# Optimization experiments

Measured on AMD Instinct MI355X. Metric: run time of the kernel, lower is better.

## Reference

```python
import jax, jax.numpy as jnp
import numpy as np

N = 16384            # mesh vertices at full resolution (level 3)
DEG = 8              # avg nonzeros per Laplacian row
F_IN = 3
F_HID = 128
LOCAL_LAYERS = 15
LEVEL_N = [N >> (3 - l) for l in range(4)]  # [2048, 4096, 8192, 16384]


def setup_inputs():
    key = jax.random.key(0)
    ks = iter(jax.random.split(key, 48))
    d = {}
    d['inputs'] = jax.random.normal(next(ks), (1, N, F_IN), dtype=jnp.float32)
    d['mask0'] = jnp.ones((1, N, 1), jnp.float32)
    d['mask1'] = jnp.ones((1, N, 1), jnp.float32)
    for l, n in enumerate(LEVEL_N):
        e = DEG * n
        d[f'lap{l}_rows'] = jnp.sort(jax.random.randint(next(ks), (e,), 0, n, dtype=jnp.int32))
        d[f'lap{l}_cols'] = jax.random.randint(next(ks), (e,), 0, n, dtype=jnp.int32)
        d[f'lap{l}_vals'] = 0.25 * jax.random.normal(next(ks), (e,), dtype=jnp.float32)
    e = DEG * N
    d['L_rows'] = jnp.sort(jax.random.randint(next(ks), (e,), 0, N, dtype=jnp.int32))
    d['L_cols'] = jax.random.randint(next(ks), (e,), 0, N, dtype=jnp.int32)
    d['L_vals'] = 0.25 * jax.random.normal(next(ks), (e,), dtype=jnp.float32)
    s_in = 0.577   # ~1/sqrt(F_IN)
    s_h = 0.0625   # 1/sqrt(2*F_HID)
    d['g_conv1_W'] = s_in * jax.random.normal(next(ks), (F_IN, F_HID), dtype=jnp.float32)
    d['g_conv1_b'] = jnp.zeros((F_HID,), jnp.float32)
    d['g_down_W'] = s_h * jax.random.normal(next(ks), (3, 2, 2 * F_HID, F_HID), dtype=jnp.float32)
    d['g_down_b'] = jnp.zeros((3, 2, F_HID), jnp.float32)
    d['g_lap0_W'] = s_h * jax.random.normal(next(ks), (2, 2 * F_HID, F_HID), dtype=jnp.float32)
    d['g_lap0_b'] = jnp.zeros((2, F_HID), jnp.float32)
    d['g_up_W'] = s_h * jax.random.normal(next(ks), (3, 2, 2 * F_HID, F_HID), dtype=jnp.float32)
    d['g_up_b'] = jnp.zeros((3, 2, F_HID), jnp.float32)
    d['g_conv2_W'] = s_h * jax.random.normal(next(ks), (F_HID, 2), dtype=jnp.float32)
    d['g_conv2_b'] = jnp.zeros((2,), jnp.float32)
    d['l_conv1_W'] = s_in * jax.random.normal(next(ks), (F_IN, F_HID), dtype=jnp.float32)
    d['l_conv1_b'] = jnp.zeros((F_HID,), jnp.float32)
    d['l_rn_W'] = s_h * jax.random.normal(next(ks), (LOCAL_LAYERS, 2, 2 * F_HID, F_HID), dtype=jnp.float32)
    d['l_rn_b'] = jnp.zeros((LOCAL_LAYERS, 2, F_HID), jnp.float32)
    d['l_conv2_W'] = s_h * jax.random.normal(next(ks), (F_HID, 1), dtype=jnp.float32)
    d['l_conv2_b'] = jnp.zeros((1,), jnp.float32)
    return d


def _spmm(rows, cols, vals, x):
    # y = L @ x for an n x n COO Laplacian; x: [1, n, f] (batch=1, sparse mm path)
    y = jax.ops.segment_sum(vals[:, None] * x[0, cols, :], rows, num_segments=x.shape[1])
    return y[None]


def _lap_block(lap, x, Ws, bs):
    # _LapResNet2 (num_outputs == num_inputs == 128): elu -> cat([x, Lx]) -> 1x1 conv, residual
    inp = x
    for j in range(Ws.shape[0]):
        x = jax.nn.elu(x)
        x = jnp.concatenate([x, _spmm(lap[0], lap[1], lap[2], x)], axis=-1) @ Ws[j] + bs[j]
    return x + inp


def _avg_block(mask, x, Ws, bs):
    # _AvgResNet2: elu -> cat([x, masked global average]) -> 1x1 conv, residual
    inp = x
    denom = jnp.sum(mask, axis=1, keepdims=True)
    for j in range(Ws.shape[0]):
        x = jax.nn.elu(x)
        avg = jnp.sum(x * mask, axis=1, keepdims=True) / denom
        x = jnp.concatenate([x, jnp.broadcast_to(avg, x.shape)], axis=-1) @ Ws[j] + bs[j]
    return x + inp


def _maxpool2(x):
    # MaxPool1d(2, stride=2) along the node dim
    b, n, f = x.shape
    return x.reshape(b, n // 2, 2, f).max(axis=2)


def _forward(inputs, mask0, mask1, lap0_vals, lap1_vals, lap2_vals, lap3_vals, L_vals,
             g_conv1_W, g_conv1_b, g_down_W, g_down_b, g_lap0_W, g_lap0_b,
             g_up_W, g_up_b, g_conv2_W, g_conv2_b,
             l_conv1_W, l_conv1_b, l_rn_W, l_rn_b, l_conv2_W, l_conv2_b,
             lap0_rows, lap0_cols, lap1_rows, lap1_cols, lap2_rows, lap2_cols,
             lap3_rows, lap3_cols, L_rows, L_cols):
    laps = [(lap0_rows, lap0_cols, lap0_vals), (lap1_rows, lap1_cols, lap1_vals),
            (lap2_rows, lap2_cols, lap2_vals), (lap3_rows, lap3_cols, lap3_vals)]
    # ----- global net: EfficientCascade (naive max-pool cascade, 4 levels) -----
    # (mask0 is only max-pooled in torch; _LapResNet2 ignores it, so it does not affect math)
    x = inputs @ g_conv1_W + g_conv1_b
    down = []
    for k, i in enumerate((3, 2, 1)):
        down.append(x)
        x = _lap_block(laps[i], x, g_down_W[k], g_down_b[k])
        x = _maxpool2(x)
    x = _lap_block(laps[0], x, g_lap0_W, g_lap0_b)
    for i in (1, 2, 3):
        x = jnp.repeat(x, 2, axis=1)      # F.interpolate(scale_factor=2), nearest
        x = x + down[-i]                  # channels equal -> plain residual add
        x = _lap_block(laps[i], x, g_up_W[i - 1], g_up_b[i - 1])
    swg = jax.nn.elu(x) @ g_conv2_W + g_conv2_b + inputs[:, :, :2]  # + repeating_expand(inputs, 2)
    # ----- local net: LapDeepModel, 15 alternating Lap / global-avg resblocks -----
    L = (L_rows, L_cols, L_vals)
    y = inputs @ l_conv1_W + l_conv1_b
    for i in range(LOCAL_LAYERS):
        if i % 2 == 0:
            y = _lap_block(L, y, l_rn_W[i], l_rn_b[i])
        else:
            y = _avg_block(mask1, y, l_rn_W[i], l_rn_b[i])
    score_local = jax.nn.elu(y) @ l_conv2_W + l_conv2_b + inputs[:, :, :1]
    # ----- combine -----
    score_global = swg[:, :, :1]
    weight_global = jax.nn.sigmoid(swg[:, :, :-1])  # out_features=1 -> same first channel
    score_final = weight_global * score_global + (1.0 - weight_global) * score_local
    return jnp.concatenate([score_global, score_local, score_final], axis=1)


def reference(inputs, mask0, mask1, lap0_rows, lap0_cols, lap0_vals,
              lap1_rows, lap1_cols, lap1_vals, lap2_rows, lap2_cols, lap2_vals,
              lap3_rows, lap3_cols, lap3_vals, L_rows, L_cols, L_vals,
              g_conv1_W, g_conv1_b, g_down_W, g_down_b, g_lap0_W, g_lap0_b,
              g_up_W, g_up_b, g_conv2_W, g_conv2_b,
              l_conv1_W, l_conv1_b, l_rn_W, l_rn_b, l_conv2_W, l_conv2_b):
    return _forward(inputs, mask0, mask1, lap0_vals, lap1_vals, lap2_vals, lap3_vals, L_vals,
                    g_conv1_W, g_conv1_b, g_down_W, g_down_b, g_lap0_W, g_lap0_b,
                    g_up_W, g_up_b, g_conv2_W, g_conv2_b,
                    l_conv1_W, l_conv1_b, l_rn_W, l_rn_b, l_conv2_W, l_conv2_b,
                    lap0_rows, lap0_cols, lap1_rows, lap1_cols, lap2_rows, lap2_cols,
                    lap3_rows, lap3_cols, L_rows, L_cols)
```

## Files before the change

### kernel.cpp

```cpp
#include <hip/hip_runtime.h>

#define F 128
#define SPAD 136
#define NR 32

typedef __attribute__((ext_vector_type(8))) short short8;
typedef __attribute__((ext_vector_type(16))) float f32x16;
typedef unsigned long long ull;

__device__ __forceinline__ float elu_f(float x) {
    return x > 0.f ? x : __expf(x) - 1.f;
}
__device__ __forceinline__ ushort f2bf(float x) {
    unsigned u = __float_as_uint(x);
    u = (u + 0x7FFFu + ((u >> 16) & 1u)) >> 16;
    return (ushort)u;
}
__device__ __forceinline__ float bf2f(ushort u) {
    return __uint_as_float((unsigned)u << 16);
}
__device__ __forceinline__ void bfma8(float* a, float v, short8 u) {
#pragma unroll
    for (int i = 0; i < 8; ++i) a[i] += v * bf2f((ushort)u[i]);
}

struct SetupArgs {
    const float* ws0; const float* ws1; const float* ws2; const float* ws3;
    ushort* wd0; ushort* wd1; ushort* wd2; ushort* wd3;
    const int* rows0; const int* rows1; const int* rows2; const int* rows3; const int* rows4;
    int* rp0; int* rp1; int* rp2; int* rp3; int* rp4;
    const float* mask; float* den; float* acc;
    const float* in; const float* Wg; const float* bg; const float* Wl; const float* bl;
    ushort* og; ushort* eg; ushort* ol; ushort* el;
};

__global__ __launch_bounds__(256) void setup_conv1(SetupArgs s) {
    __shared__ ushort tile[16384];
    int b = blockIdx.x, t = threadIdx.x;
    if (b >= 274) {
        int id = (b - 274) * 256 + t;
        int r = id >> 7, c = id & 127;
        float x0 = s.in[r * 3 + 0], x1 = s.in[r * 3 + 1], x2 = s.in[r * 3 + 2];
        float g = x0 * s.Wg[c] + x1 * s.Wg[F + c] + x2 * s.Wg[2 * F + c] + s.bg[c];
        float lo = x0 * s.Wl[c] + x1 * s.Wl[F + c] + x2 * s.Wl[2 * F + c] + s.bl[c];
        s.og[id] = f2bf(g);  s.eg[id] = f2bf(elu_f(g));
        s.ol[id] = f2bf(lo); s.el[id] = f2bf(elu_f(lo));
    } else if (b < 88) {
        const float* src; ushort* dst; int lb;
        if (b < 12)      { src = s.ws0; dst = s.wd0; lb = b; }
        else if (b < 16) { src = s.ws1; dst = s.wd1; lb = b - 12; }
        else if (b < 28) { src = s.ws2; dst = s.wd2; lb = b - 16; }
        else             { src = s.ws3; dst = s.wd3; lb = b - 28; }
        src += (size_t)lb * 16384; dst += (size_t)lb * 16384;
        for (int idx = t; idx < 16384; idx += 256) {
            int k = idx >> 7, nn = idx & 127;
            int k0 = k >> 4, rk = k & 15, j = rk & 7, lh = rk >> 3;
            int n0 = nn >> 5, ll = nn & 31;
            tile[((k0 * 4 + n0) * 64 + lh * 32 + ll) * 8 + j] = f2bf(src[idx]);
        }
        __syncthreads();
        ull* td = (ull*)dst; const ull* ts = (const ull*)tile;
        for (int i = t; i < 4096; i += 256) td[i] = ts[i];
    } else if (b < 273) {
        int tid = (b - 88) * 256 + t;
        const int ns[5] = {2048, 4096, 8192, 16384, 16384};
        const int es[5] = {16384, 32768, 65536, 131072, 131072};
        const int* rowsA[5] = {s.rows0, s.rows1, s.rows2, s.rows3, s.rows4};
        int* rpA[5] = {s.rp0, s.rp1, s.rp2, s.rp3, s.rp4};
        int base = 0;
        for (int lv = 0; lv < 5; ++lv) {
            int cnt = ns[lv] + 1;
            if (tid < base + cnt) {
                int r = tid - base;
                const int* rows = rowsA[lv]; int e = es[lv];
                int lo = 0, hi = e;
                while (lo < hi) { int mid = (lo + hi) >> 1; if (rows[mid] < r) lo = mid + 1; else hi = mid; }
                rpA[lv][r] = lo;
                return;
            }
            base += cnt;
        }
    } else {
        __shared__ float red[256];
        float ssum = 0.f;
        for (int i = t; i < 16384; i += 256) ssum += s.mask[i];
        red[t] = ssum; __syncthreads();
        for (int st = 128; st > 0; st >>= 1) { if (t < st) red[t] += red[t + st]; __syncthreads(); }
        if (t == 0) s.den[0] = red[0];
        for (int i = t; i < 14336; i += 256) s.acc[i] = 0.f;
    }
}

struct LArgs {
    const ushort* EA; const ushort* RES; ushort* OUT; ushort* EAOUT;
    const int* rowptr; const int* cols; const float* vals;
    const ushort* Wp; const float* bias;
    const float* accin; const float* den;
    const float* mask; float* accout;
    ushort* EO; ushort* EE; const ushort* SKIP;
    int epi;
    int fin;
    const float* Finp; const ushort* FEB0;
    const float* FgW2; const float* Fgb2; const float* FlW2; const float* Flb2;
    float* Fout;
};

__device__ __forceinline__ void layer_body(const LArgs& a, int blk, ushort* SS, float* FS) {
    const int t = threadIdx.x;
    const int rbase = blk * NR;
    const int w = t >> 6, l = t & 63, m = l & 31, kh = l >> 5;
    const int col = w * 32 + m;
    const bool lap = (a.rowptr != nullptr);
    const bool avg = (a.accin != nullptr);

    if (lap) {
        const int grp = t >> 3, l8 = t & 7;
        const int lbase = (t & 63) & ~7;
        const short8* EA8 = (const short8*)a.EA;
        const int chunk = l8 * 2;
        const int row = rbase + grp;
        const int e0 = a.rowptr[row], e1 = a.rowptr[row + 1];
        float acc0[16];
#pragma unroll
        for (int i = 0; i < 16; ++i) acc0[i] = 0.f;
        int myc = 0; float myv = 0.f;
        {
            int e = e0 + l8;
            if (e < e1) { myc = a.cols[e]; myv = a.vals[e]; }
        }
#pragma unroll 1
        for (int base = e0; base < e1; base += 8) {
            int nc = 0; float nv = 0.f;
            {
                int en = base + 8 + l8;
                if (en < e1) { nc = a.cols[en]; nv = a.vals[en]; }
            }
            int cnt = e1 - base; if (cnt > 8) cnt = 8;
            int cc[8];
#pragma unroll
            for (int k = 0; k < 8; ++k) cc[k] = __shfl(myc, lbase + k, 64);
            short8 ua[8], ub[8];
#pragma unroll
            for (int k = 0; k < 8; ++k) {
                if (k < cnt) {
                    ua[k] = EA8[(size_t)cc[k] * 16 + chunk];
                    ub[k] = EA8[(size_t)cc[k] * 16 + chunk + 1];
                }
            }
#pragma unroll
            for (int k = 0; k < 8; ++k) {
                if (k < cnt) {
                    float v = __shfl(myv, lbase + k, 64);
                    bfma8(acc0, v, ua[k]);
                    bfma8(acc0 + 8, v, ub[k]);
                }
            }
            myc = nc; myv = nv;
        }
        short8 s0, s1;
#pragma unroll
        for (int i = 0; i < 8; ++i) {
            s0[i] = (short)f2bf(acc0[i]);
            s1[i] = (short)f2bf(acc0[8 + i]);
        }
        *(short8*)(&SS[grp * SPAD + l8 * 16]) = s0;
        *(short8*)(&SS[grp * SPAD + l8 * 16 + 8]) = s1;
        __syncthreads();
    } else if (avg) {
        if (t < 128) {
            float s = 0.f;
#pragma unroll
            for (int r = 0; r < 8; ++r) s += a.accin[r * 128 + t];
            SS[t] = f2bf(s / a.den[0]);
        }
        __syncthreads();
    }

    short8 afrag[8];
    {
        const ushort* ear = a.EA + (size_t)(rbase + m) * F + kh * 8;
#pragma unroll
        for (int ki = 0; ki < 8; ++ki) afrag[ki] = *(const short8*)(ear + ki * 16);
    }

    f32x16 acc;
#pragma unroll
    for (int i = 0; i < 16; ++i) acc[i] = 0.f;
#pragma unroll
    for (int ki = 0; ki < 8; ++ki) {
        short8 b = *(const short8*)(a.Wp + (size_t)(((ki * 4 + w) * 64 + l) * 8));
        acc = __builtin_amdgcn_mfma_f32_32x32x16_bf16(afrag[ki], b, acc, 0, 0, 0);
    }
    if (lap || avg) {
        const ushort* esr = lap ? &SS[m * SPAD + kh * 8] : &SS[kh * 8];
#pragma unroll
        for (int ki = 0; ki < 8; ++ki) {
            short8 aa = *(const short8*)(esr + ki * 16);
            short8 b = *(const short8*)(a.Wp + 16384 + (size_t)(((ki * 4 + w) * 64 + l) * 8));
            acc = __builtin_amdgcn_mfma_f32_32x32x16_bf16(aa, b, acc, 0, 0, 0);
        }
    }

    const float bv = a.bias[col];
    float outv[16];
#pragma unroll
    for (int reg = 0; reg < 16; ++reg) {
        int r = (reg & 3) + 8 * (reg >> 2) + 4 * kh;
        size_t rg = (size_t)(rbase + r);
        float v = acc[reg] + bv;
        if (a.RES) v += bf2f(a.RES[rg * F + col]);
        outv[reg] = v;
        if (a.OUT) a.OUT[rg * F + col] = f2bf(v);
        if (a.EAOUT) a.EAOUT[rg * F + col] = f2bf(elu_f(v));
    }
    if (a.accout) {
        float p = 0.f;
#pragma unroll
        for (int reg = 0; reg < 16; ++reg) {
            int r = (reg & 3) + 8 * (reg >> 2) + 4 * kh;
            p += elu_f(outv[reg]) * a.mask[rbase + r];
        }
        p += __shfl_xor(p, 32, 64);
        if (l < 32) atomicAdd(a.accout + (blk & 7) * 128 + col, p);
    }
    if (a.epi == 1) {
        int rb2 = rbase >> 1;
#pragma unroll
        for (int q = 0; q < 4; ++q)
#pragma unroll
            for (int e2 = 0; e2 < 2; ++e2) {
                float pv = fmaxf(outv[q * 4 + e2 * 2], outv[q * 4 + e2 * 2 + 1]);
                size_t idx = (size_t)(rb2 + q * 4 + kh * 2 + e2) * F + col;
                a.EO[idx] = f2bf(pv);
                a.EE[idx] = f2bf(elu_f(pv));
            }
    } else if (a.epi == 2) {
#pragma unroll
        for (int reg = 0; reg < 16; ++reg) {
            int r = (reg & 3) + 8 * (reg >> 2) + 4 * kh;
            size_t R0 = (size_t)(2 * (rbase + r)) * F + col;
            float v0 = outv[reg] + bf2f(a.SKIP[R0]);
            float v1 = outv[reg] + bf2f(a.SKIP[R0 + F]);
            a.EO[R0] = f2bf(v0);     a.EO[R0 + F] = f2bf(v1);
            a.EE[R0] = f2bf(elu_f(v0)); a.EE[R0 + F] = f2bf(elu_f(v1));
        }
    }
    if (a.fin) {
        __syncthreads();
        if (t < 64) FS[t] = 0.f;
        __syncthreads();
        const float lw = a.FlW2[col];
#pragma unroll
        for (int reg = 0; reg < 16; ++reg) {
            int r = (reg & 3) + 8 * (reg >> 2) + 4 * kh;
            atomicAdd(&FS[r], elu_f(outv[reg]) * lw);
        }
        for (int idx = t; idx < 32 * 128; idx += 256) {
            int r = idx >> 7, cc = idx & 127;
            atomicAdd(&FS[32 + r], bf2f(a.FEB0[(size_t)(rbase + r) * F + cc]) * a.FgW2[2 * cc]);
        }
        __syncthreads();
        if (t < 32) {
            int rg = rbase + t;
            float base = a.Finp[rg * 3 + 0];
            float sg = FS[32 + t] + a.Fgb2[0] + base;
            float sl = FS[t] + a.Flb2[0] + base;
            float wg = 1.f / (1.f + __expf(-sg));
            a.Fout[rg] = sg;
            a.Fout[16384 + rg] = sl;
            a.Fout[32768 + rg] = wg * sg + (1.f - wg) * sl;
        }
    }
}

__global__ __launch_bounds__(256)
void dual_layer(LArgs A, LArgs B, int nA) {
    __shared__ ushort SS[NR * SPAD];
    __shared__ float FS[64];
    bool isA = (int)blockIdx.x < nA;
    const LArgs& a = isA ? A : B;
    int blk = isA ? blockIdx.x : blockIdx.x - nA;
    layer_body(a, blk, SS, FS);
}

extern "C" void kernel_launch(void* const* d_in, const int* in_sizes, int n_in,
                              void* d_out, int out_size, void* d_ws, size_t ws_size,
                              hipStream_t stream) {
    (void)in_sizes; (void)n_in; (void)out_size; (void)ws_size;
    const float* inputs = (const float*)d_in[0];
    const float* mask1  = (const float*)d_in[2];
    const int*   lrows[5] = {(const int*)d_in[3], (const int*)d_in[6], (const int*)d_in[9],
                             (const int*)d_in[12], (const int*)d_in[15]};
    const int*   lcols[5] = {(const int*)d_in[4], (const int*)d_in[7], (const int*)d_in[10],
                             (const int*)d_in[13], (const int*)d_in[16]};
    const float* lvals[5] = {(const float*)d_in[5], (const float*)d_in[8], (const float*)d_in[11],
                             (const float*)d_in[14], (const float*)d_in[17]};
    const float* gW1 = (const float*)d_in[18];
    const float* gb1 = (const float*)d_in[19];
    const float* gdW = (const float*)d_in[20];
    const float* gdb = (const float*)d_in[21];
    const float* glW = (const float*)d_in[22];
    const float* glb = (const float*)d_in[23];
    const float* guW = (const float*)d_in[24];
    const float* gub = (const float*)d_in[25];
    const float* gW2 = (const float*)d_in[26];
    const float* gb2 = (const float*)d_in[27];
    const float* lW1 = (const float*)d_in[28];
    const float* lb1 = (const float*)d_in[29];
    const float* lrW = (const float*)d_in[30];
    const float* lrb = (const float*)d_in[31];
    const float* lW2 = (const float*)d_in[32];
    const float* lb2 = (const float*)d_in[33];
    float* out = (float*)d_out;

    const int N = 16384;
    const int nlev[5] = {2048, 4096, 8192, 16384, 16384};

    char* ws = (char*)d_ws;
    size_t off = 0;
    auto alloc = [&](size_t bytes) -> char* {
        char* p = ws + off;
        off = (off + bytes + 255) & ~(size_t)255;
        return p;
    };
    ushort* BUF0 = (ushort*)alloc((size_t)N * F * 2);
    ushort* GU2  = (ushort*)alloc((size_t)N * F * 2);
    ushort* G2   = (ushort*)alloc((size_t)N * F * 2);
    ushort* D8   = (ushort*)alloc((size_t)8192 * F * 2);
    ushort* D4   = (ushort*)alloc((size_t)4096 * F * 2);
    ushort* D2   = (ushort*)alloc((size_t)2048 * F * 2);
    ushort* LB   = (ushort*)alloc((size_t)N * F * 2);
    ushort* EB0 = (ushort*)alloc((size_t)N * F * 2);
    ushort* EG1 = (ushort*)alloc((size_t)N * F * 2);
    ushort* EG2 = (ushort*)alloc((size_t)N * F * 2);
    ushort* ED8 = (ushort*)alloc((size_t)8192 * F * 2);
    ushort* ED4 = (ushort*)alloc((size_t)4096 * F * 2);
    ushort* ED2 = (ushort*)alloc((size_t)2048 * F * 2);
    ushort* LE1 = (ushort*)alloc((size_t)N * F * 2);
    ushort* LE2 = (ushort*)alloc((size_t)N * F * 2);
    int* rp[5];
    for (int i = 0; i < 5; ++i) rp[i] = (int*)alloc((size_t)(nlev[i] + 1) * 4);
    float* ACC = (float*)alloc((size_t)14 * 8 * 128 * 4);
    float* DEN = (float*)alloc(4);
    ushort* Pd = (ushort*)alloc((size_t)12 * 16384 * 2);
    ushort* Pl = (ushort*)alloc((size_t)4  * 16384 * 2);
    ushort* Pu = (ushort*)alloc((size_t)12 * 16384 * 2);
    ushort* Pr = (ushort*)alloc((size_t)60 * 16384 * 2);

    SetupArgs sa;
    sa.ws0 = gdW; sa.ws1 = glW; sa.ws2 = guW; sa.ws3 = lrW;
    sa.wd0 = Pd;  sa.wd1 = Pl;  sa.wd2 = Pu;  sa.wd3 = Pr;
    sa.rows0 = lrows[0]; sa.rows1 = lrows[1]; sa.rows2 = lrows[2];
    sa.rows3 = lrows[3]; sa.rows4 = lrows[4];
    sa.rp0 = rp[0]; sa.rp1 = rp[1]; sa.rp2 = rp[2]; sa.rp3 = rp[3]; sa.rp4 = rp[4];
    sa.mask = mask1; sa.den = DEN; sa.acc = ACC;
    sa.in = inputs; sa.Wg = gW1; sa.bg = gb1; sa.Wl = lW1; sa.bl = lb1;
    sa.og = BUF0; sa.eg = EB0; sa.ol = LB; sa.el = LE1;
    setup_conv1<<<274 + 8192, 256, 0, stream>>>(sa);

    const size_t PSZ = 2 * 16384;

    auto mkL = [&](const ushort* ea, const ushort* res, ushort* o, ushort* eao,
                   int lv, const ushort* wp, const float* bias, float* accout,
                   int epi, ushort* eo, ushort* ee, const ushort* skip,
                   const float* accin, int fin) {
        LArgs x;
        x.EA = ea; x.RES = res; x.OUT = o; x.EAOUT = eao;
        x.rowptr = (lv >= 0) ? rp[lv] : nullptr;
        x.cols = (lv >= 0) ? lcols[lv] : nullptr;
        x.vals = (lv >= 0) ? lvals[lv] : nullptr;
        x.Wp = wp; x.bias = bias;
        x.accin = accin; x.den = DEN;
        x.mask = mask1; x.accout = accout;
        x.EO = eo; x.EE = ee; x.SKIP = skip; x.epi = epi;
        x.fin = fin;
        x.Finp = inputs; x.FEB0 = EB0;
        x.FgW2 = gW2; x.Fgb2 = gb2; x.FlW2 = lW2; x.Flb2 = lb2; x.Fout = out;
        return x;
    };

    LArgs gs[14]; int gn[14];
    gs[0]  = mkL(EB0, 0, 0, EG1, 3, Pd + 0 * PSZ, gdb + 0,   0, 0, 0, 0, 0, 0, 0);  gn[0]  = 16384;
    gs[1]  = mkL(EG1, BUF0, 0, 0, 3, Pd + 1 * PSZ, gdb + 128, 0, 1, D8, ED8, 0, 0, 0); gn[1] = 16384;
    gs[2]  = mkL(ED8, 0, 0, EG1, 2, Pd + 2 * PSZ, gdb + 256, 0, 0, 0, 0, 0, 0, 0);  gn[2]  = 8192;
    gs[3]  = mkL(EG1, D8, 0, 0, 2, Pd + 3 * PSZ, gdb + 384, 0, 1, D4, ED4, 0, 0, 0); gn[3]  = 8192;
    gs[4]  = mkL(ED4, 0, 0, EG1, 1, Pd + 4 * PSZ, gdb + 512, 0, 0, 0, 0, 0, 0, 0);  gn[4]  = 4096;
    gs[5]  = mkL(EG1, D4, 0, 0, 1, Pd + 5 * PSZ, gdb + 640, 0, 1, D2, ED2, 0, 0, 0); gn[5]  = 4096;
    gs[6]  = mkL(ED2, 0, 0, EG1, 0, Pl + 0 * PSZ, glb + 0,   0, 0, 0, 0, 0, 0, 0);  gn[6]  = 2048;
    gs[7]  = mkL(EG1, D2, 0, 0, 0, Pl + 1 * PSZ, glb + 128, 0, 2, GU2, EG2, D4, 0, 0); gn[7] = 2048;
    gs[8]  = mkL(EG2, 0, 0, EG1, 1, Pu + 0 * PSZ, gub + 0,   0, 0, 0, 0, 0, 0, 0);  gn[8]  = 4096;
    gs[9]  = mkL(EG1, GU2, 0, 0, 1, Pu + 1 * PSZ, gub + 128, 0, 2, G2, EG2, D8, 0, 0); gn[9] = 4096;
    gs[10] = mkL(EG2, 0, 0, EG1, 2, Pu + 2 * PSZ, gub + 256, 0, 0, 0, 0, 0, 0, 0);  gn[10] = 8192;
    gs[11] = mkL(EG1, G2, 0, 0, 2, Pu + 3 * PSZ, gub + 384, 0, 2, GU2, EG2, BUF0, 0, 0); gn[11] = 8192;
    gs[12] = mkL(EG2, 0, 0, EG1, 3, Pu + 4 * PSZ, gub + 512, 0, 0, 0, 0, 0, 0, 0);  gn[12] = 16384;
    gs[13] = mkL(EG1, GU2, 0, EB0, 3, Pu + 5 * PSZ, gub + 640, 0, 0, 0, 0, 0, 0, 0); gn[13] = 16384;

    int gi = 0;
    auto launchLap = [&](const LArgs& loc) {
        if (gi < 14) {
            int na = gn[gi] / NR;
            dual_layer<<<na + 512, 256, 0, stream>>>(gs[gi], loc, na);
            ++gi;
        } else {
            dual_layer<<<512, 256, 0, stream>>>(loc, loc, 512);
        }
    };

    for (int i = 0; i < 15; ++i) {
        const ushort* P1 = Pr + (size_t)(2 * i) * PSZ;
        const ushort* P2 = Pr + (size_t)(2 * i + 1) * PSZ;
        const float* b1 = lrb + (size_t)i * 256;
        const float* b2 = b1 + 128;
        if ((i & 1) == 0) {
            LArgs s1 = mkL(LE1, 0, 0, LE2, 4, P1, b1, 0, 0, 0, 0, 0, 0, 0);
            float* accout = (i <= 12) ? (ACC + (size_t)i * 1024) : nullptr;
            int fin = (i == 14);
            LArgs s2 = mkL(LE2, LB, fin ? nullptr : LB, fin ? nullptr : LE1, 4,
                           P2, b2, accout, 0, 0, 0, 0, 0, fin);
            launchLap(s1);
            launchLap(s2);
        } else {
            LArgs s1 = mkL(LE1, 0, 0, LE2, -1, P1, b1, ACC + (size_t)i * 1024,
                           0, 0, 0, 0, ACC + (size_t)(i - 1) * 1024, 0);
            LArgs s2 = mkL(LE2, LB, LB, LE1, -1, P2, b2, 0,
                           0, 0, 0, 0, ACC + (size_t)i * 1024, 0);
            launchLap(s1);
            launchLap(s2);
        }
    }
}
```

Baseline: 646.7 us.

## Halve rows per block and switch to 16x16x32 MFMA tiles

Rows per block drop from 32 to 16, so each layer launches twice as many blocks. The weight pre-pack layout and the GEMM are rewritten to use 16x16x32 bf16 MFMA with two column tiles per wave instead of one 32x32x16 tile. The sparse gather now uses 16 lanes per row, each loading one 8-element chunk. The goal is more parallelism and more latency hiding for the memory-bound SpMM and GEMM stages, at the cost of more redundant weight loads per row and more per-block overhead.

```diff
diff --git a/kernel.cpp b/kernel.cpp
--- a/kernel.cpp
+++ b/kernel.cpp
@@ -2,10 +2,10 @@
 
 #define F 128
 #define SPAD 136
-#define NR 32
+#define NR 16
 
 typedef __attribute__((ext_vector_type(8))) short short8;
-typedef __attribute__((ext_vector_type(16))) float f32x16;
+typedef __attribute__((ext_vector_type(4))) float f32x4;
 typedef unsigned long long ull;
 
 __device__ __forceinline__ float elu_f(float x) {
@@ -54,9 +54,9 @@
         src += (size_t)lb * 16384; dst += (size_t)lb * 16384;
         for (int idx = t; idx < 16384; idx += 256) {
             int k = idx >> 7, nn = idx & 127;
-            int k0 = k >> 4, rk = k & 15, j = rk & 7, lh = rk >> 3;
-            int n0 = nn >> 5, ll = nn & 31;
-            tile[((k0 * 4 + n0) * 64 + lh * 32 + ll) * 8 + j] = f2bf(src[idx]);
+            int kt = k >> 5, lq = (k >> 3) & 3, j = k & 7;
+            int wv = nn >> 5, ct = (nn >> 4) & 1, cc = nn & 15;
+            tile[((((kt * 4 + wv) * 2 + ct) * 64 + lq * 16 + cc)) * 8 + j] = f2bf(src[idx]);
         }
         __syncthreads();
         ull* td = (ull*)dst; const ull* ts = (const ull*)tile;
@@ -108,63 +108,55 @@
 __device__ __forceinline__ void layer_body(const LArgs& a, int blk, ushort* SS, float* FS) {
     const int t = threadIdx.x;
     const int rbase = blk * NR;
-    const int w = t >> 6, l = t & 63, m = l & 31, kh = l >> 5;
-    const int col = w * 32 + m;
+    const int w = t >> 6, l = t & 63;
+    const int cl = l & 15, lq = l >> 4;
     const bool lap = (a.rowptr != nullptr);
     const bool avg = (a.accin != nullptr);
 
     if (lap) {
-        const int grp = t >> 3, l8 = t & 7;
-        const int lbase = (t & 63) & ~7;
+        const int grp = t >> 4, l16 = t & 15;
+        const int lbase = l & ~15;
         const short8* EA8 = (const short8*)a.EA;
-        const int chunk = l8 * 2;
         const int row = rbase + grp;
         const int e0 = a.rowptr[row], e1 = a.rowptr[row + 1];
-        float acc0[16];
-#pragma unroll
-        for (int i = 0; i < 16; ++i) acc0[i] = 0.f;
+        float acc0[8];
+#pragma unroll
+        for (int i = 0; i < 8; ++i) acc0[i] = 0.f;
         int myc = 0; float myv = 0.f;
-        {
-            int e = e0 + l8;
-            if (e < e1) { myc = a.cols[e]; myv = a.vals[e]; }
-        }
+        if (e0 + l16 < e1) { myc = a.cols[e0 + l16]; myv = a.vals[e0 + l16]; }
 #pragma unroll 1
-        for (int base = e0; base < e1; base += 8) {
+        for (int base = e0; base < e1; base += 16) {
             int nc = 0; float nv = 0.f;
             {
-                int en = base + 8 + l8;
+                int en = base + 16 + l16;
                 if (en < e1) { nc = a.cols[en]; nv = a.vals[en]; }
             }
-            int cnt = e1 - base; if (cnt > 8) cnt = 8;
-            int cc[8];
-#pragma unroll
-            for (int k = 0; k < 8; ++k) cc[k] = __shfl(myc, lbase + k, 64);
-            short8 ua[8], ub[8];
-#pragma unroll
-            for (int k = 0; k < 8; ++k) {
-                if (k < cnt) {
-                    ua[k] = EA8[(size_t)cc[k] * 16 + chunk];
-                    ub[k] = EA8[(size_t)cc[k] * 16 + chunk + 1];
-                }
-            }
-#pragma unroll
-            for (int k = 0; k < 8; ++k) {
-                if (k < cnt) {
-                    float v = __shfl(myv, lbase + k, 64);
-                    bfma8(acc0, v, ua[k]);
-                    bfma8(acc0 + 8, v, ub[k]);
+#pragma unroll
+            for (int half = 0; half < 2; ++half) {
+                int hb = base + half * 8;
+                if (hb < e1) {
+                    int cnt = e1 - hb; if (cnt > 8) cnt = 8;
+                    int cc[8];
+#pragma unroll
+                    for (int k = 0; k < 8; ++k) cc[k] = __shfl(myc, lbase + half * 8 + k, 64);
+                    short8 ua[8];
+#pragma unroll
+                    for (int k = 0; k < 8; ++k)
+                        if (k < cnt) ua[k] = EA8[(size_t)cc[k] * 16 + l16];
+#pragma unroll
+                    for (int k = 0; k < 8; ++k)
+                        if (k < cnt) {
+                            float v = __shfl(myv, lbase + half * 8 + k, 64);
+                            bfma8(acc0, v, ua[k]);
+                        }
                 }
             }
             myc = nc; myv = nv;
         }
-        short8 s0, s1;
-#pragma unroll
-        for (int i = 0; i < 8; ++i) {
-            s0[i] = (short)f2bf(acc0[i]);
-            s1[i] = (short)f2bf(acc0[8 + i]);
-        }
-        *(short8*)(&SS[grp * SPAD + l8 * 16]) = s0;
-        *(short8*)(&SS[grp * SPAD + l8 * 16 + 8]) = s1;
+        short8 s0;
+#pragma unroll
+        for (int i = 0; i < 8; ++i) s0[i] = (short)f2bf(acc0[i]);
+        *(short8*)(&SS[grp * SPAD + l16 * 8]) = s0;
         __syncthreads();
     } else if (avg) {
         if (t < 128) {
@@ -176,94 +168,108 @@
         __syncthreads();
     }
 
-    short8 afrag[8];
+    short8 afrag[4];
     {
-        const ushort* ear = a.EA + (size_t)(rbase + m) * F + kh * 8;
-#pragma unroll
-        for (int ki = 0; ki < 8; ++ki) afrag[ki] = *(const short8*)(ear + ki * 16);
-    }
-
-    f32x16 acc;
-#pragma unroll
-    for (int i = 0; i < 16; ++i) acc[i] = 0.f;
-#pragma unroll
-    for (int ki = 0; ki < 8; ++ki) {
-        short8 b = *(const short8*)(a.Wp + (size_t)(((ki * 4 + w) * 64 + l) * 8));
-        acc = __builtin_amdgcn_mfma_f32_32x32x16_bf16(afrag[ki], b, acc, 0, 0, 0);
+        const ushort* ear = a.EA + (size_t)(rbase + cl) * F + lq * 8;
+#pragma unroll
+        for (int kt = 0; kt < 4; ++kt) afrag[kt] = *(const short8*)(ear + kt * 32);
+    }
+
+    f32x4 accA, accB;
+#pragma unroll
+    for (int i = 0; i < 4; ++i) { accA[i] = 0.f; accB[i] = 0.f; }
+#pragma unroll
+    for (int kt = 0; kt < 4; ++kt) {
+        short8 b0 = *(const short8*)(a.Wp + (size_t)((((kt * 4 + w) * 2 + 0) * 64 + l) * 8));
+        short8 b1 = *(const short8*)(a.Wp + (size_t)((((kt * 4 + w) * 2 + 1) * 64 + l) * 8));
+        accA = __builtin_amdgcn_mfma_f32_16x16x32_bf16(afrag[kt], b0, accA, 0, 0, 0);
+        accB = __builtin_amdgcn_mfma_f32_16x16x32_bf16(afrag[kt], b1, accB, 0, 0, 0);
     }
     if (lap || avg) {
-        const ushort* esr = lap ? &SS[m * SPAD + kh * 8] : &SS[kh * 8];
-#pragma unroll
-        for (int ki = 0; ki < 8; ++ki) {
-            short8 aa = *(const short8*)(esr + ki * 16);
-            short8 b = *(const short8*)(a.Wp + 16384 + (size_t)(((ki * 4 + w) * 64 + l) * 8));
-            acc = __builtin_amdgcn_mfma_f32_32x32x16_bf16(aa, b, acc, 0, 0, 0);
-        }
-    }
-
-    const float bv = a.bias[col];
-    float outv[16];
-#pragma unroll
-    for (int reg = 0; reg < 16; ++reg) {
-        int r = (reg & 3) + 8 * (reg >> 2) + 4 * kh;
+        const ushort* esr = lap ? &SS[cl * SPAD + lq * 8] : &SS[lq * 8];
+#pragma unroll
+        for (int kt = 0; kt < 4; ++kt) {
+            short8 aa = *(const short8*)(esr + kt * 32);
+            short8 b0 = *(const short8*)(a.Wp + 16384 + (size_t)((((kt * 4 + w) * 2 + 0) * 64 + l) * 8));
+            short8 b1 = *(const short8*)(a.Wp + 16384 + (size_t)((((kt * 4 + w) * 2 + 1) * 64 + l) * 8));
+            accA = __builtin_amdgcn_mfma_f32_16x16x32_bf16(aa, b0, accA, 0, 0, 0);
+            accB = __builtin_amdgcn_mfma_f32_16x16x32_bf16(aa, b1, accB, 0, 0, 0);
+        }
+    }
+
+    const int col0 = w * 32 + cl, col1 = w * 32 + 16 + cl;
+    const float bv0 = a.bias[col0], bv1 = a.bias[col1];
+    float outv[8];
+#pragma unroll
+    for (int reg = 0; reg < 4; ++reg) {
+        int r = lq * 4 + reg;
         size_t rg = (size_t)(rbase + r);
-        float v = acc[reg] + bv;
-        if (a.RES) v += bf2f(a.RES[rg * F + col]);
-        outv[reg] = v;
-        if (a.OUT) a.OUT[rg * F + col] = f2bf(v);
-        if (a.EAOUT) a.EAOUT[rg * F + col] = f2bf(elu_f(v));
+        float v0 = accA[reg] + bv0;
+        float v1 = accB[reg] + bv1;
+        if (a.RES) { v0 += bf2f(a.RES[rg * F + col0]); v1 += bf2f(a.RES[rg * F + col1]); }
+        outv[reg] = v0; outv[4 + reg] = v1;
+        if (a.OUT) { a.OUT[rg * F + col0] = f2bf(v0); a.OUT[rg * F + col1] = f2bf(v1); }
+        if (a.EAOUT) { a.EAOUT[rg * F + col0] = f2bf(elu_f(v0)); a.EAOUT[rg * F + col1] = f2bf(elu_f(v1)); }
     }
     if (a.accout) {
-        float p = 0.f;
-#pragma unroll
-        for (int reg = 0; reg < 16; ++reg) {
-            int r = (reg & 3) + 8 * (reg >> 2) + 4 * kh;
-            p += elu_f(outv[reg]) * a.mask[rbase + r];
-        }
-        p += __shfl_xor(p, 32, 64);
-        if (l < 32) atomicAdd(a.accout + (blk & 7) * 128 + col, p);
+        float p0 = 0.f, p1 = 0.f;
+#pragma unroll
+        for (int reg = 0; reg < 4; ++reg) {
+            float mk = a.mask[rbase + lq * 4 + reg];
+            p0 += elu_f(outv[reg]) * mk;
+            p1 += elu_f(outv[4 + reg]) * mk;
+        }
+        p0 += __shfl_xor(p0, 16, 64); p0 += __shfl_xor(p0, 32, 64);
+        p1 += __shfl_xor(p1, 16, 64); p1 += __shfl_xor(p1, 32, 64);
+        if (l < 16) {
+            atomicAdd(a.accout + (blk & 7) * 128 + w * 32 + l, p0);
+            atomicAdd(a.accout + (blk & 7) * 128 + w * 32 + 16 + l, p1);
+        }
     }
     if (a.epi == 1) {
         int rb2 = rbase >> 1;
 #pragma unroll
-        for (int q = 0; q < 4; ++q)
+        for (int ct = 0; ct < 2; ++ct)
 #pragma unroll
             for (int e2 = 0; e2 < 2; ++e2) {
-                float pv = fmaxf(outv[q * 4 + e2 * 2], outv[q * 4 + e2 * 2 + 1]);
-                size_t idx = (size_t)(rb2 + q * 4 + kh * 2 + e2) * F + col;
+                float pv = fmaxf(outv[ct * 4 + e2 * 2], outv[ct * 4 + e2 * 2 + 1]);
+                size_t idx = (size_t)(rb2 + lq * 2 + e2) * F + (ct ? col1 : col0);
                 a.EO[idx] = f2bf(pv);
                 a.EE[idx] = f2bf(elu_f(pv));
             }
     } else if (a.epi == 2) {
 #pragma unroll
-        for (int reg = 0; reg < 16; ++reg) {
-            int r = (reg & 3) + 8 * (reg >> 2) + 4 * kh;
-            size_t R0 = (size_t)(2 * (rbase + r)) * F + col;
-            float v0 = outv[reg] + bf2f(a.SKIP[R0]);
-            float v1 = outv[reg] + bf2f(a.SKIP[R0 + F]);
-            a.EO[R0] = f2bf(v0);     a.EO[R0 + F] = f2bf(v1);
-            a.EE[R0] = f2bf(elu_f(v0)); a.EE[R0 + F] = f2bf(elu_f(v1));
-        }
+        for (int ct = 0; ct < 2; ++ct)
+#pragma unroll
+            for (int reg = 0; reg < 4; ++reg) {
+                int r = lq * 4 + reg;
+                size_t R0 = (size_t)(2 * (rbase + r)) * F + (ct ? col1 : col0);
+                float v0 = outv[ct * 4 + reg] + bf2f(a.SKIP[R0]);
+                float v1 = outv[ct * 4 + reg] + bf2f(a.SKIP[R0 + F]);
+                a.EO[R0] = f2bf(v0);     a.EO[R0 + F] = f2bf(v1);
+                a.EE[R0] = f2bf(elu_f(v0)); a.EE[R0 + F] = f2bf(elu_f(v1));
+            }
     }
     if (a.fin) {
         __syncthreads();
-        if (t < 64) FS[t] = 0.f;
-        __syncthreads();
-        const float lw = a.FlW2[col];
-#pragma unroll
-        for (int reg = 0; reg < 16; ++reg) {
-            int r = (reg & 3) + 8 * (reg >> 2) + 4 * kh;
-            atomicAdd(&FS[r], elu_f(outv[reg]) * lw);
-        }
-        for (int idx = t; idx < 32 * 128; idx += 256) {
+        if (t < 32) FS[t] = 0.f;
+        __syncthreads();
+#pragma unroll
+        for (int ct = 0; ct < 2; ++ct) {
+            float lw = a.FlW2[ct ? col1 : col0];
+#pragma unroll
+            for (int reg = 0; reg < 4; ++reg)
+                atomicAdd(&FS[lq * 4 + reg], elu_f(outv[ct * 4 + reg]) * lw);
+        }
+        for (int idx = t; idx < 16 * 128; idx += 256) {
             int r = idx >> 7, cc = idx & 127;
-            atomicAdd(&FS[32 + r], bf2f(a.FEB0[(size_t)(rbase + r) * F + cc]) * a.FgW2[2 * cc]);
-        }
-        __syncthreads();
-        if (t < 32) {
+            atomicAdd(&FS[16 + r], bf2f(a.FEB0[(size_t)(rbase + r) * F + cc]) * a.FgW2[2 * cc]);
+        }
+        __syncthreads();
+        if (t < 16) {
             int rg = rbase + t;
             float base = a.Finp[rg * 3 + 0];
-            float sg = FS[32 + t] + a.Fgb2[0] + base;
+            float sg = FS[16 + t] + a.Fgb2[0] + base;
             float sl = FS[t] + a.Flb2[0] + base;
             float wg = 1.f / (1.f + __expf(-sg));
             a.Fout[rg] = sg;
@@ -395,14 +401,15 @@
     gs[12] = mkL(EG2, 0, 0, EG1, 3, Pu + 4 * PSZ, gub + 512, 0, 0, 0, 0, 0, 0, 0);  gn[12] = 16384;
     gs[13] = mkL(EG1, GU2, 0, EB0, 3, Pu + 5 * PSZ, gub + 640, 0, 0, 0, 0, 0, 0, 0); gn[13] = 16384;
 
+    const int NB_LOC = N / NR;
     int gi = 0;
     auto launchLap = [&](const LArgs& loc) {
         if (gi < 14) {
             int na = gn[gi] / NR;
-            dual_layer<<<na + 512, 256, 0, stream>>>(gs[gi], loc, na);
+            dual_layer<<<na + NB_LOC, 256, 0, stream>>>(gs[gi], loc, na);
             ++gi;
         } else {
-            dual_layer<<<512, 256, 0, stream>>>(loc, loc, 512);
+            dual_layer<<<NB_LOC, 256, 0, stream>>>(loc, loc, NB_LOC);
         }
     };
 
```

Result: faster. 596.0 us (median of 2 runs) (-7.8%).
